# Kernel optimization log

Hardware: AMD Instinct MI355X
Metric: run time of the kernel (lower is better)

Reference implementation:

```python
import jax, jax.numpy as jnp
import numpy as np

NEIGHBOR_NUM = 16
POOLING_RATE = 4


def setup_inputs() -> dict:
    key = jax.random.key(0)
    k1, k2, k3 = jax.random.split(key, 3)
    bs, v, c = 16, 2048, 512
    vertices = jax.random.normal(k1, (bs, v, 3), dtype=jnp.float32)
    feature_map = jax.random.normal(k2, (bs, v, c), dtype=jnp.float32)
    pool_num = v // POOLING_RATE  # 512
    sample_idx = jax.random.randint(k3, (pool_num,), 0, v, dtype=jnp.int32)
    return {"vertices": vertices, "feature_map": feature_map, "sample_idx": sample_idx}


def _get_neighbor_index(vertices, neighbor_num):
    # vertices: (bs, v, 3) -> (bs, v, neighbor_num)
    inner = jnp.einsum("bnd,bmd->bnm", vertices, vertices)  # (bs, v, v)
    quadratic = jnp.sum(vertices * vertices, axis=2)  # (bs, v)
    distance = -2.0 * inner + quadratic[:, None, :] + quadratic[:, :, None]
    k = min(neighbor_num + 1, vertices.shape[1])
    # smallest-k == top-k of negated distance; drop self (first column)
    _, idx = jax.lax.top_k(-distance, k)  # (bs, v, k)
    return idx[:, :, 1:]


def reference(vertices, feature_map, sample_idx):
    neighbor_index = _get_neighbor_index(vertices, NEIGHBOR_NUM)  # (bs, v, n)
    # gather per-batch: (bs, v, n, c)
    neighbor_feature = jax.vmap(lambda f, i: f[i])(feature_map, neighbor_index)
    pooled_feature = jnp.max(neighbor_feature, axis=2)  # (bs, v, c)
    vertices_pool = vertices[:, sample_idx, :]  # (bs, pool_num, 3)
    feature_map_pool = pooled_feature[:, sample_idx, :]  # (bs, pool_num, c)
    return (vertices_pool, feature_map_pool)
```

## Files before the change

kernel.cpp:

```cpp
#include <hip/hip_runtime.h>

#define BS 16
#define V  2048
#define C  512
#define PN 512
#define K  16
#define NT 256

typedef unsigned long long u64;
typedef unsigned int u32;

template<int CTRL>
__device__ __forceinline__ u32 min_dpp_u32(u32 x) {
    const u32 n = (u32)__builtin_amdgcn_update_dpp((int)x, (int)x, CTRL, 0xF, 0xF, false);
    return n < x ? n : x;
}
__device__ __forceinline__ u32 wave_min_u32(u32 x) {
    x = min_dpp_u32<0x111>(x);
    x = min_dpp_u32<0x112>(x);
    x = min_dpp_u32<0x114>(x);
    x = min_dpp_u32<0x118>(x);
    x = min_dpp_u32<0x142>(x);
    x = min_dpp_u32<0x143>(x);
    return (u32)__builtin_amdgcn_readlane((int)x, 63);
}
__device__ __forceinline__ int mbcnt64(u64 m) {
    return __builtin_amdgcn_mbcnt_hi((u32)(m >> 32),
           __builtin_amdgcn_mbcnt_lo((u32)m, 0));
}

#define CE(i, j) { const bool p_ = sk[j] < sk[i]; const u64 a_ = p_ ? sk[j] : sk[i]; \
                   const u64 b_ = p_ ? sk[i] : sk[j]; sk[i] = a_; sk[j] = b_; }

__global__ __launch_bounds__(NT) void pool_knn_kernel(
    const float* __restrict__ vert,
    const float* __restrict__ feat,
    const int*   __restrict__ sidx,
    float* __restrict__ out)
{
    const int blk = blockIdx.x;
    const int b = blk >> 9;
    const int s = blk & (PN - 1);
    const int t = threadIdx.x;
    const int wid = t >> 6;
    const int lane = t & 63;
    const u32 wbase = (u32)wid * 512u;

    const int q = sidx[s];
    const float* vb = vert + (size_t)b * (V * 3);
    const float qx = vb[q * 3 + 0];
    const float qy = vb[q * 3 + 1];
    const float qz = vb[q * 3 + 2];
    const float qq = qx * qx + qy * qy + qz * qz;

    __shared__ u64 wlist[(NT / 64) * K];
    __shared__ int nbr[K];

    u32 d0, d1, d2, d3, d4, d5, d6, d7, perm;
    {
        u64 sk[8];
        #pragma unroll
        for (int i = 0; i < 8; ++i) {
            const int m = (int)wbase + i * 64 + lane;
            const float mx = vb[m * 3 + 0];
            const float my = vb[m * 3 + 1];
            const float mz = vb[m * 3 + 2];
            const float qm = mx * mx + my * my + mz * mz;
            const float inner = qx * mx + qy * my + qz * mz;
            const float dist = (-2.0f * inner + qm) + qq;
            u32 u = __float_as_uint(dist);
            u ^= (u & 0x80000000u) ? 0xFFFFFFFFu : 0x80000000u;
            if (m == q) u = 0xFFFFFFFFu;
            sk[i] = ((u64)u << 32) | (u32)i;
        }
        CE(0,1) CE(2,3) CE(4,5) CE(6,7)
        CE(0,2) CE(1,3) CE(4,6) CE(5,7)
        CE(1,2) CE(5,6) CE(0,4) CE(3,7)
        CE(1,5) CE(2,6)
        CE(1,4) CE(3,6)
        CE(2,4) CE(3,5)
        CE(3,4)
        d0 = (u32)(sk[0] >> 32); d1 = (u32)(sk[1] >> 32);
        d2 = (u32)(sk[2] >> 32); d3 = (u32)(sk[3] >> 32);
        d4 = (u32)(sk[4] >> 32); d5 = (u32)(sk[5] >> 32);
        d6 = (u32)(sk[6] >> 32); d7 = (u32)(sk[7] >> 32);
        perm = (u32)sk[0]        | ((u32)sk[1] << 4)  | ((u32)sk[2] << 8)  |
               ((u32)sk[3] << 12)| ((u32)sk[4] << 16) | ((u32)sk[5] << 20) |
               ((u32)sk[6] << 24)| ((u32)sk[7] << 28);
    }

    {
        int r = 0;
        while (r < K) {
            const u32 wm = wave_min_u32(d0);
            const bool pred = (d0 == wm);
            const u64 mask = __ballot(pred);
            const int cnt = (int)__popcll(mask);
            const u64 hid = __ballot(d1 == wm);
            if ((r + cnt <= K) && (hid == 0ull)) {
                if (pred) {
                    const u32 idx = wbase + ((perm & 15u) << 6) + (u32)lane;
                    wlist[wid * K + r + mbcnt64(mask)] = ((u64)d0 << 32) | idx;
                }
                d0 = pred ? d1 : d0; d1 = pred ? d2 : d1; d2 = pred ? d3 : d2;
                d3 = pred ? d4 : d3; d4 = pred ? d5 : d4; d5 = pred ? d6 : d5;
                d6 = pred ? d7 : d6; d7 = pred ? 0xFFFFFFFFu : d7;
                perm = pred ? (perm >> 4) : perm;
                r += cnt;
            } else {
                const u32 myidx = pred ? (wbase + ((perm & 15u) << 6) + (u32)lane)
                                       : 0xFFFFFFFFu;
                const u32 wi = wave_min_u32(myidx);
                const bool w2 = pred && (myidx == wi);
                if (w2) wlist[wid * K + r] = ((u64)d0 << 32) | myidx;
                d0 = w2 ? d1 : d0; d1 = w2 ? d2 : d1; d2 = w2 ? d3 : d2;
                d3 = w2 ? d4 : d3; d4 = w2 ? d5 : d4; d5 = w2 ? d6 : d5;
                d6 = w2 ? d7 : d6; d7 = w2 ? 0xFFFFFFFFu : d7;
                perm = w2 ? (perm >> 4) : perm;
                r += 1;
            }
        }
    }
    __syncthreads();

    if (wid == 0) {
        const u64 ck = wlist[lane];
        u32 cd = (u32)(ck >> 32);
        const u32 ci = (u32)ck;
        int r = 0;
        while (r < K) {
            const u32 wm = wave_min_u32(cd);
            const bool pred = (cd == wm);
            const u64 mask = __ballot(pred);
            const int cnt = (int)__popcll(mask);
            if (r + cnt <= K) {
                if (pred) nbr[r + mbcnt64(mask)] = (int)ci;
                cd = pred ? 0xFFFFFFFFu : cd;
                r += cnt;
            } else {
                const u32 mi = pred ? ci : 0xFFFFFFFFu;
                const u32 wi = wave_min_u32(mi);
                const bool w2 = pred && (ci == wi);
                if (w2) nbr[r] = (int)ci;
                cd = w2 ? 0xFFFFFFFFu : cd;
                r += 1;
            }
        }
    }
    __syncthreads();

    const float* fb = feat + (size_t)b * (V * C);
    const int ch = t * 2;
    float m0 = -__builtin_inff(), m1 = -__builtin_inff();
    #pragma unroll
    for (int r = 0; r < K; ++r) {
        const int idx = __builtin_amdgcn_readfirstlane(nbr[r]);
        const float2 f = *reinterpret_cast<const float2*>(fb + (size_t)idx * C + ch);
        m0 = fmaxf(m0, f.x);
        m1 = fmaxf(m1, f.y);
    }
    float* o1 = out + (size_t)BS * PN * 3 + (size_t)(b * PN + s) * C + ch;
    o1[0] = m0;
    o1[1] = m1;

    if (t < 3) {
        out[(size_t)(b * PN + s) * 3 + t] = vb[q * 3 + t];
    }
}

extern "C" void kernel_launch(void* const* d_in, const int* in_sizes, int n_in,
                              void* d_out, int out_size, void* d_ws, size_t ws_size,
                              hipStream_t stream) {
    const float* vert = (const float*)d_in[0];
    const float* feat = (const float*)d_in[1];
    const int*   sidx = (const int*)d_in[2];
    float* out = (float*)d_out;

    pool_knn_kernel<<<BS * PN, NT, 0, stream>>>(vert, feat, sidx, out);
}
```

Before: 143.1 us.

## Pop top-8 per wave, merge via bitonic swizzle, refine only when needed

Each wave now extracts only its 8 smallest candidates with a fixed unrolled pop sequence instead of 16. The four sorted lists are merged with a ds_swizzle bitonic network to get a tentative global top-16. A fallback pass pops extra candidates and rerun the serial wave-0 merge only if some wave's 8th element is below the 16th global key. This is meant to cut the serial wave-min/ballot extraction work per block, at the cost of added branching, extra syncs and a slow path that is rarely taken.

After: 129.8 us. 1.1x faster.

```diff
diff --git a/kernel.cpp b/kernel.cpp
--- a/kernel.cpp
+++ b/kernel.cpp
@@ -24,6 +24,28 @@
     x = min_dpp_u32<0x143>(x);
     return (u32)__builtin_amdgcn_readlane((int)x, 63);
 }
+template<int CTRL>
+__device__ __forceinline__ u64 max_dpp_u64(u64 x) {
+    const int lo = (int)(u32)x, hi = (int)(u32)(x >> 32);
+    const int plo = __builtin_amdgcn_update_dpp(lo, lo, CTRL, 0xF, 0xF, false);
+    const int phi = __builtin_amdgcn_update_dpp(hi, hi, CTRL, 0xF, 0xF, false);
+    const u64 p = ((u64)(u32)phi << 32) | (u32)plo;
+    return p > x ? p : x;
+}
+template<int OFS>
+__device__ __forceinline__ u64 swz_u64(u64 x) {
+    const int lo = __builtin_amdgcn_ds_swizzle((int)(u32)x, OFS);
+    const int hi = __builtin_amdgcn_ds_swizzle((int)(u32)(x >> 32), OFS);
+    return ((u64)(u32)hi << 32) | (u32)lo;
+}
+template<int D, int OFS>
+__device__ __forceinline__ u64 bitonic_stage(u64 x, int ll) {
+    const u64 p = swz_u64<OFS>(x);
+    const bool keepmin = ((ll & D) == 0);
+    const bool pl = (p < x);
+    const bool takep = keepmin ? pl : !pl;
+    return takep ? p : x;
+}
 __device__ __forceinline__ int mbcnt64(u64 m) {
     return __builtin_amdgcn_mbcnt_hi((u32)(m >> 32),
            __builtin_amdgcn_mbcnt_lo((u32)m, 0));
@@ -31,6 +53,32 @@
 
 #define CE(i, j) { const bool p_ = sk[j] < sk[i]; const u64 a_ = p_ ? sk[j] : sk[i]; \
                    const u64 b_ = p_ ? sk[i] : sk[j]; sk[i] = a_; sk[j] = b_; }
+
+#define POP_ONE(SLOT)                                                          \
+    {                                                                          \
+        const u32 wm = wave_min_u32(d0);                                       \
+        const bool pred = (d0 == wm);                                          \
+        const u64 mask = __ballot(pred);                                       \
+        const int cnt = (int)__popcll(mask);                                   \
+        const u64 hid = __ballot(d1 == wm);                                    \
+        bool w_;                                                               \
+        if ((cnt == 1) && (hid == 0ull)) {                                     \
+            w_ = pred;                                                         \
+        } else {                                                               \
+            const u32 myidx = pred ? (wbase + ((perm & 15u) << 6) + (u32)lane) \
+                                   : 0xFFFFFFFFu;                              \
+            const u32 wi = wave_min_u32(myidx);                                \
+            w_ = pred && (myidx == wi);                                        \
+        }                                                                      \
+        if (w_) {                                                              \
+            const u32 idx = wbase + ((perm & 15u) << 6) + (u32)lane;           \
+            wlist[wid * 16 + (SLOT)] = ((u64)d0 << 32) | idx;                  \
+        }                                                                      \
+        d0 = w_ ? d1 : d0; d1 = w_ ? d2 : d1; d2 = w_ ? d3 : d2;               \
+        d3 = w_ ? d4 : d3; d4 = w_ ? d5 : d4; d5 = w_ ? d6 : d5;               \
+        d6 = w_ ? d7 : d6; d7 = w_ ? 0xFFFFFFFFu : d7;                         \
+        perm = w_ ? (perm >> 4) : perm;                                        \
+    }
 
 __global__ __launch_bounds__(NT) void pool_knn_kernel(
     const float* __restrict__ vert,
@@ -46,15 +94,19 @@
     const int lane = t & 63;
     const u32 wbase = (u32)wid * 512u;
 
+    __shared__ u64 wlist[64];
+    __shared__ int nbr[K];
+    __shared__ int flagw;
+    __shared__ int cntw[4];
+    if (t == 0) flagw = 0;
+    if (t < 4) cntw[t] = 8;
+
     const int q = sidx[s];
     const float* vb = vert + (size_t)b * (V * 3);
     const float qx = vb[q * 3 + 0];
     const float qy = vb[q * 3 + 1];
     const float qz = vb[q * 3 + 2];
     const float qq = qx * qx + qy * qy + qz * qz;
-
-    __shared__ u64 wlist[(NT / 64) * K];
-    __shared__ int nbr[K];
 
     u32 d0, d1, d2, d3, d4, d5, d6, d7, perm;
     {
@@ -89,73 +141,97 @@
                ((u32)sk[6] << 24)| ((u32)sk[7] << 28);
     }
 
+    #pragma unroll
+    for (int r = 0; r < 8; ++r) { POP_ONE(r) }
+    __syncthreads();
+
+    u64 x;
     {
-        int r = 0;
-        while (r < K) {
-            const u32 wm = wave_min_u32(d0);
-            const bool pred = (d0 == wm);
-            const u64 mask = __ballot(pred);
-            const int cnt = (int)__popcll(mask);
-            const u64 hid = __ballot(d1 == wm);
-            if ((r + cnt <= K) && (hid == 0ull)) {
-                if (pred) {
-                    const u32 idx = wbase + ((perm & 15u) << 6) + (u32)lane;
-                    wlist[wid * K + r + mbcnt64(mask)] = ((u64)d0 << 32) | idx;
+        const int w = lane >> 3;
+        const int rr = (w & 1) ? (7 - (lane & 7)) : (lane & 7);
+        const int addr = (w & 3) * 16 + rr;
+        const u64 ld = wlist[(lane < 32) ? addr : 0];
+        x = (lane < 32) ? ld : ~0ULL;
+        const int ll = lane & 15;
+        x = bitonic_stage<8, 0x201F>(x, ll);
+        x = bitonic_stage<4, 0x101F>(x, ll);
+        x = bitonic_stage<2, 0x081F>(x, ll);
+        x = bitonic_stage<1, 0x041F>(x, ll);
+        const u64 p = swz_u64<0x7C1F>(x);
+        x = (p < x) ? p : x;
+    }
+
+    u64 B16;
+    {
+        u64 bm = (lane < 16) ? x : 0ULL;
+        bm = max_dpp_u64<0x121>(bm);
+        bm = max_dpp_u64<0x122>(bm);
+        bm = max_dpp_u64<0x124>(bm);
+        bm = max_dpp_u64<0x128>(bm);
+        const u32 blo = (u32)__builtin_amdgcn_readlane((int)(u32)bm, 0);
+        const u32 bhi = (u32)__builtin_amdgcn_readlane((int)(u32)(bm >> 32), 0);
+        B16 = ((u64)bhi << 32) | blo;
+    }
+    const u64 k8 = wlist[wid * 16 + 7];
+    const int resu = __builtin_amdgcn_readfirstlane((int)(k8 < B16));
+    if (resu && lane == 0) flagw = 1;
+    __syncthreads();
+
+    int nidx[K];
+    if (flagw != 0) {
+        if (resu) {
+            int r = 8;
+            while (r < 16) {
+                const u32 fm = wave_min_u32(d0);
+                if (((u64)fm << 32) > B16) break;
+                POP_ONE(r)
+                ++r;
+            }
+            if (lane == 0) cntw[wid] = r;
+        }
+        __syncthreads();
+        if (wid == 0) {
+            const int cv = cntw[lane >> 4];
+            const u64 ck = ((lane & 15) < cv) ? wlist[lane] : ~0ULL;
+            u32 cd = (u32)(ck >> 32);
+            const u32 ci = (u32)ck;
+            int r = 0;
+            while (r < K) {
+                const u32 wm = wave_min_u32(cd);
+                const bool pred = (cd == wm);
+                const u64 mask = __ballot(pred);
+                const int cnt = (int)__popcll(mask);
+                if (r + cnt <= K) {
+                    if (pred) nbr[r + mbcnt64(mask)] = (int)ci;
+                    cd = pred ? 0xFFFFFFFFu : cd;
+                    r += cnt;
+                } else {
+                    const u32 mi = pred ? ci : 0xFFFFFFFFu;
+                    const u32 wi = wave_min_u32(mi);
+                    const bool w2 = pred && (ci == wi);
+                    if (w2) nbr[r] = (int)ci;
+                    cd = w2 ? 0xFFFFFFFFu : cd;
+                    r += 1;
                 }
-                d0 = pred ? d1 : d0; d1 = pred ? d2 : d1; d2 = pred ? d3 : d2;
-                d3 = pred ? d4 : d3; d4 = pred ? d5 : d4; d5 = pred ? d6 : d5;
-                d6 = pred ? d7 : d6; d7 = pred ? 0xFFFFFFFFu : d7;
-                perm = pred ? (perm >> 4) : perm;
-                r += cnt;
-            } else {
-                const u32 myidx = pred ? (wbase + ((perm & 15u) << 6) + (u32)lane)
-                                       : 0xFFFFFFFFu;
-                const u32 wi = wave_min_u32(myidx);
-                const bool w2 = pred && (myidx == wi);
-                if (w2) wlist[wid * K + r] = ((u64)d0 << 32) | myidx;
-                d0 = w2 ? d1 : d0; d1 = w2 ? d2 : d1; d2 = w2 ? d3 : d2;
-                d3 = w2 ? d4 : d3; d4 = w2 ? d5 : d4; d5 = w2 ? d6 : d5;
-                d6 = w2 ? d7 : d6; d7 = w2 ? 0xFFFFFFFFu : d7;
-                perm = w2 ? (perm >> 4) : perm;
-                r += 1;
             }
         }
-    }
-    __syncthreads();
-
-    if (wid == 0) {
-        const u64 ck = wlist[lane];
-        u32 cd = (u32)(ck >> 32);
-        const u32 ci = (u32)ck;
-        int r = 0;
-        while (r < K) {
-            const u32 wm = wave_min_u32(cd);
-            const bool pred = (cd == wm);
-            const u64 mask = __ballot(pred);
-            const int cnt = (int)__popcll(mask);
-            if (r + cnt <= K) {
-                if (pred) nbr[r + mbcnt64(mask)] = (int)ci;
-                cd = pred ? 0xFFFFFFFFu : cd;
-                r += cnt;
-            } else {
-                const u32 mi = pred ? ci : 0xFFFFFFFFu;
-                const u32 wi = wave_min_u32(mi);
-                const bool w2 = pred && (ci == wi);
-                if (w2) nbr[r] = (int)ci;
-                cd = w2 ? 0xFFFFFFFFu : cd;
-                r += 1;
-            }
-        }
-    }
-    __syncthreads();
+        __syncthreads();
+        #pragma unroll
+        for (int r = 0; r < K; ++r)
+            nidx[r] = __builtin_amdgcn_readfirstlane(nbr[r]);
+    } else {
+        const int xlo = (int)(u32)x;
+        #pragma unroll
+        for (int r = 0; r < K; ++r)
+            nidx[r] = __builtin_amdgcn_readlane(xlo, r);
+    }
 
     const float* fb = feat + (size_t)b * (V * C);
     const int ch = t * 2;
     float m0 = -__builtin_inff(), m1 = -__builtin_inff();
     #pragma unroll
     for (int r = 0; r < K; ++r) {
-        const int idx = __builtin_amdgcn_readfirstlane(nbr[r]);
-        const float2 f = *reinterpret_cast<const float2*>(fb + (size_t)idx * C + ch);
+        const float2 f = *reinterpret_cast<const float2*>(fb + (size_t)nidx[r] * C + ch);
         m0 = fmaxf(m0, f.x);
         m1 = fmaxf(m1, f.y);
     }
```
